# Performance work log

Hardware: AMD Instinct MI355X
Metric: run time of the kernel (lower is better)

The kernel has to match this reference:

```python
import jax, jax.numpy as jnp
import numpy as np

N = 50000   # nodes
E = 800000  # edges
C = 64      # num_channels
EPS = 1e-5


def setup_inputs() -> dict:
    key = jax.random.key(0)
    ks = jax.random.split(key, 12)
    x = jax.random.normal(ks[0], (N, C), dtype=jnp.float32)
    vec = jax.random.normal(ks[1], (N, 3, C), dtype=jnp.float32)
    senders = jax.random.randint(ks[2], (E,), 0, N, dtype=jnp.int32)
    receivers = jax.random.randint(ks[3], (E,), 0, N, dtype=jnp.int32)
    interaction_matrices = jax.random.normal(ks[4], (E, 3, 3), dtype=jnp.float32)
    # learned parameters
    ln_scale = jnp.ones((C,), dtype=jnp.float32)
    ln_bias = jnp.zeros((C,), dtype=jnp.float32)
    vln_weight = jnp.ones((C,), dtype=jnp.float32)  # VecLayerNorm weight (norm_type='none' -> identity norm, channel scale)
    w1 = jax.random.normal(ks[5], (C, 2 * C), dtype=jnp.float32) / np.sqrt(C)
    b1 = jnp.zeros((2 * C,), dtype=jnp.float32)
    w2 = jax.random.normal(ks[6], (2 * C, C), dtype=jnp.float32) / np.sqrt(2 * C)
    b2 = jnp.zeros((C,), dtype=jnp.float32)
    return {
        "x": x, "vec": vec, "senders": senders, "receivers": receivers,
        "interaction_matrices": interaction_matrices,
        "ln_scale": ln_scale, "ln_bias": ln_bias, "vln_weight": vln_weight,
        "w1": w1, "b1": b1, "w2": w2, "b2": b2,
    }


def reference(x, vec, senders, receivers, interaction_matrices,
              ln_scale, ln_bias, vln_weight, w1, b1, w2, b2):
    # LayerNorm(eps=1e-5) over channel dim
    mean = jnp.mean(x, axis=-1, keepdims=True)
    var = jnp.var(x, axis=-1, keepdims=True)
    x_norm = (x - mean) * jax.lax.rsqrt(var + EPS) * ln_scale + ln_bias
    # VecLayerNorm with norm_type='none': identity norm, learned per-channel weight
    vec_norm = vec * vln_weight  # [N, 3, C]
    # MLP: Dense(2C) -> silu -> Dense(C)
    p = jax.nn.silu(x_norm @ w1 + b1) @ w2 + b2  # [N, C]
    # gather to edges
    p_i = p[receivers]            # [E, C]
    p_j = p[senders]              # [E, C]
    vec_i = vec_norm[receivers]   # [E, 3, C]
    vec_j = vec_norm[senders]     # [E, 3, C]
    source_dipole = p_j[:, None, :] * vec_j                              # [E, 3, C]
    field_at_i = jnp.einsum('eij,ejc->eic', interaction_matrices, source_dipole)  # [E, 3, C]
    dEnergy = jnp.sum(p_i[:, None, :] * vec_i * field_at_i, axis=1)      # [E, C]
    dx = jax.ops.segment_sum(dEnergy, receivers, num_segments=x.shape[0])  # [N, C]
    return dx
```

## Files before the change

### kernel.cpp

```cpp
#include <hip/hip_runtime.h>

#define C 64
#define EPS 1e-5f
#define BUCK_CAP 1536
#define OVF_CAP 65536
#define SMASK 0x03ffffffu

typedef __attribute__((ext_vector_type(8))) short bf16x8;
typedef __attribute__((ext_vector_type(4))) float f32x4;

static __device__ __forceinline__ unsigned int f2bf(float f) {
  unsigned int x = __float_as_uint(f);
  return (x + 0x7fffu + ((x >> 16) & 1u)) >> 16;
}
static __device__ __forceinline__ float bflo2f(unsigned int p) {
  return __uint_as_float(p << 16);
}
static __device__ __forceinline__ float bfhi2f(unsigned int p) {
  return __uint_as_float(p & 0xffff0000u);
}

__global__ __launch_bounds__(256) void prep_weights(
    const float* __restrict__ w1, const float* __restrict__ w2,
    unsigned short* __restrict__ w1T, unsigned short* __restrict__ w2T) {
  int idx = blockIdx.x * 256 + threadIdx.x;
  if (idx < 2 * C * C) {
    int k = idx >> 6, c = idx & 63;
    w1T[idx] = (unsigned short)f2bf(w1[c * 2 * C + k]);
  } else if (idx < 4 * C * C) {
    int j = idx - 2 * C * C;
    int c = j >> 7, k = j & 127;
    w2T[j] = (unsigned short)f2bf(w2[k * C + c]);
  }
}

__global__ __launch_bounds__(256) void bin_kernel(
    const int* __restrict__ recv, const int* __restrict__ send,
    uint2* __restrict__ region, int* __restrict__ bucketCnt,
    int* __restrict__ ovfList, int* __restrict__ ovfCnt,
    int n_edges, int nbuck) {
  __shared__ int hist[1024];
  int t = threadIdx.x;
  for (int i = t; i < 1024; i += 256) hist[i] = 0;
  __syncthreads();

  int base = blockIdx.x * 4096;
  int myrecv[16], mysend[16];
#pragma unroll 16
  for (int j = 0; j < 16; j++) {
    int e = base + j * 256 + t;
    if (e < n_edges) {
      int r = recv[e];
      myrecv[j] = r;
      mysend[j] = send[e];
      atomicAdd(&hist[r >> 6], 1);
    } else {
      myrecv[j] = -1;
      mysend[j] = 0;
    }
  }
  __syncthreads();

  for (int i = t; i < nbuck; i += 256) {
    int c = hist[i];
    hist[i] = (c > 0) ? atomicAdd(&bucketCnt[i], c) : 0;
  }
  __syncthreads();

#pragma unroll 16
  for (int j = 0; j < 16; j++) {
    int r = myrecv[j];
    if (r >= 0) {
      int e = base + j * 256 + t;
      int b = r >> 6;
      int pos = atomicAdd(&hist[b], 1);
      if (pos < BUCK_CAP) {
        uint2 rec;
        rec.x = (unsigned)mysend[j] | ((unsigned)(r & 63) << 26);
        rec.y = (unsigned)e;
        region[(size_t)b * BUCK_CAP + pos] = rec;
      } else {
        int o = atomicAdd(ovfCnt, 1);
        if (o < OVF_CAP) ovfList[o] = e;
      }
    }
  }
}

__global__ __launch_bounds__(256) void sort_kernel(
    uint2* __restrict__ region, const int* __restrict__ bucketCnt,
    int* __restrict__ nodeBeg, int* __restrict__ nodeEnd, int n_nodes) {
  __shared__ uint2 buf[BUCK_CAP];
  __shared__ int hist[64];
  __shared__ int off[64];
  int b = blockIdx.x;
  int t = threadIdx.x;
  int cnt = bucketCnt[b];
  if (cnt > BUCK_CAP) cnt = BUCK_CAP;
  uint2* reg = region + (size_t)b * BUCK_CAP;

  if (t < 64) hist[t] = 0;
  __syncthreads();
  for (int i = t; i < cnt; i += 256) {
    uint2 r = reg[i];
    buf[i] = r;
    atomicAdd(&hist[r.x >> 26], 1);
  }
  __syncthreads();
  if (t == 0) {
    int run = 0;
#pragma unroll
    for (int j = 0; j < 64; j++) { off[j] = run; run += hist[j]; }
  }
  __syncthreads();
  for (int i = t; i < cnt; i += 256) {
    uint2 r = buf[i];
    int pos = atomicAdd(&off[r.x >> 26], 1);
    reg[pos] = r;
  }
  __syncthreads();
  if (t < 64) {
    int node = b * 64 + t;
    if (node < n_nodes) {
      int end = off[t];
      nodeBeg[node] = b * BUCK_CAP + (end - hist[t]);
      nodeEnd[node] = b * BUCK_CAP + end;
    }
  }
}

__global__ __launch_bounds__(256, 2) void node_kernel(
    const float* __restrict__ x, const float* __restrict__ vec,
    const float* __restrict__ ln_scale, const float* __restrict__ ln_bias,
    const float* __restrict__ vln_w,
    const unsigned short* __restrict__ w1T, const float* __restrict__ b1,
    const unsigned short* __restrict__ w2T, const float* __restrict__ b2,
    uint2* __restrict__ D16, int n_nodes) {
  __shared__ unsigned short An[64 * 72];
  __shared__ unsigned short Ss[64 * 136];
  __shared__ unsigned short W1s[128 * 72];
  __shared__ unsigned short W2s[64 * 136];

  const int t = threadIdx.x;
  const int lane = t & 63;
  const int wave = t >> 6;
  const int l15 = lane & 15;
  const int q = lane >> 4;

  {
    int r1 = t >> 1, h2 = t & 1;
    const uint4* s1 = (const uint4*)(w1T + r1 * 64 + h2 * 32);
    uint4* d1 = (uint4*)(W1s + r1 * 72 + h2 * 32);
    d1[0] = s1[0]; d1[1] = s1[1]; d1[2] = s1[2]; d1[3] = s1[3];
    int r2 = t >> 2, qd = t & 3;
    const uint4* s2 = (const uint4*)(w2T + r2 * 128 + qd * 32);
    uint4* d2 = (uint4*)(W2s + r2 * 136 + qd * 32);
    d2[0] = s2[0]; d2[1] = s2[1]; d2[2] = s2[2]; d2[3] = s2[3];
  }

  {
    int rowl = t >> 2;
    int part = t & 3;
    int node = blockIdx.x * 64 + rowl;
    int nc = node < n_nodes ? node : n_nodes - 1;
    const float* xp = x + (size_t)nc * C + part * 16;
    float xv[16];
    float s = 0.f;
#pragma unroll
    for (int i = 0; i < 4; i++) {
      float4 v = *(const float4*)(xp + i * 4);
      xv[i * 4 + 0] = v.x; xv[i * 4 + 1] = v.y;
      xv[i * 4 + 2] = v.z; xv[i * 4 + 3] = v.w;
      s += v.x + v.y + v.z + v.w;
    }
    s += __shfl_xor(s, 1);
    s += __shfl_xor(s, 2);
    float mean = s * (1.f / C);
    float vs = 0.f;
#pragma unroll
    for (int i = 0; i < 16; i++) {
      float d = xv[i] - mean;
      vs += d * d;
    }
    vs += __shfl_xor(vs, 1);
    vs += __shfl_xor(vs, 2);
    float rs = rsqrtf(vs * (1.f / C) + EPS);
    float ls[16], lb[16];
#pragma unroll
    for (int i = 0; i < 4; i++) {
      float4 a = *(const float4*)(ln_scale + part * 16 + i * 4);
      float4 b = *(const float4*)(ln_bias + part * 16 + i * 4);
      ls[i * 4 + 0] = a.x; ls[i * 4 + 1] = a.y; ls[i * 4 + 2] = a.z; ls[i * 4 + 3] = a.w;
      lb[i * 4 + 0] = b.x; lb[i * 4 + 1] = b.y; lb[i * 4 + 2] = b.z; lb[i * 4 + 3] = b.w;
    }
    unsigned int bp[8];
#pragma unroll
    for (int i = 0; i < 8; i++) {
      float e0 = (xv[2 * i] - mean) * rs * ls[2 * i] + lb[2 * i];
      float e1 = (xv[2 * i + 1] - mean) * rs * ls[2 * i + 1] + lb[2 * i + 1];
      bp[i] = f2bf(e0) | (f2bf(e1) << 16);
    }
    uint4* dst = (uint4*)(An + rowl * 72 + part * 16);
    uint4 p0 = {bp[0], bp[1], bp[2], bp[3]};
    uint4 p1 = {bp[4], bp[5], bp[6], bp[7]};
    dst[0] = p0;
    dst[1] = p1;
  }
  __syncthreads();

  const int Mbase = wave * 16;

  bf16x8 a0 = *(const bf16x8*)(An + (Mbase + l15) * 72 + q * 8);
  bf16x8 a1 = *(const bf16x8*)(An + (Mbase + l15) * 72 + 32 + q * 8);
  f32x4 acc1[8];
#pragma unroll
  for (int nt = 0; nt < 8; nt++) {
    const unsigned short* wb = W1s + (nt * 16 + l15) * 72 + q * 8;
    bf16x8 b0 = *(const bf16x8*)(wb);
    bf16x8 b1f = *(const bf16x8*)(wb + 32);
    f32x4 z = {0.f, 0.f, 0.f, 0.f};
    z = __builtin_amdgcn_mfma_f32_16x16x32_bf16(a0, b0, z, 0, 0, 0);
    z = __builtin_amdgcn_mfma_f32_16x16x32_bf16(a1, b1f, z, 0, 0, 0);
    acc1[nt] = z;
  }
#pragma unroll
  for (int nt = 0; nt < 8; nt++) {
    float bb = b1[nt * 16 + l15];
#pragma unroll
    for (int r = 0; r < 4; r++) {
      float h = acc1[nt][r] + bb;
      float sg = h / (1.f + __expf(-h));
      Ss[(Mbase + q * 4 + r) * 136 + nt * 16 + l15] = (unsigned short)f2bf(sg);
    }
  }
  __syncthreads();

  bf16x8 a2[4];
#pragma unroll
  for (int kt = 0; kt < 4; kt++)
    a2[kt] = *(const bf16x8*)(Ss + (Mbase + l15) * 136 + kt * 32 + q * 8);
  f32x4 acc2[4];
#pragma unroll
  for (int nt = 0; nt < 4; nt++) {
    f32x4 z = {0.f, 0.f, 0.f, 0.f};
#pragma unroll
    for (int kt = 0; kt < 4; kt++) {
      bf16x8 b = *(const bf16x8*)(W2s + (nt * 16 + l15) * 136 + kt * 32 + q * 8);
      z = __builtin_amdgcn_mfma_f32_16x16x32_bf16(a2[kt], b, z, 0, 0, 0);
    }
    acc2[nt] = z;
  }

#pragma unroll
  for (int nt = 0; nt < 4; nt++) {
    int cc = nt * 16 + l15;
    float bb = b2[cc];
    float vw = vln_w[cc];
#pragma unroll
    for (int r = 0; r < 4; r++) {
      int rl = Mbase + q * 4 + r;
      int nn = blockIdx.x * 64 + rl;
      if (nn < n_nodes) {
        float p = (acc2[nt][r] + bb) * vw;
        const float* vp = vec + (size_t)nn * (3 * C) + cc;
        float v0 = vp[0], v1 = vp[C], v2 = vp[2 * C];
        uint2 u;
        u.x = f2bf(p * v0) | (f2bf(p * v1) << 16);
        u.y = f2bf(p * v2);
        D16[(size_t)nn * C + cc] = u;
      }
    }
  }
}

__global__ __launch_bounds__(256) void accum_node(
    const uint2* __restrict__ region, const int* __restrict__ nodeBeg,
    const int* __restrict__ nodeEnd, const float* __restrict__ Mmat,
    const uint2* __restrict__ D2, float* __restrict__ dx, int n_nodes) {
  int wid = threadIdx.x >> 6;
  int lane = threadIdx.x & 63;
  int n = blockIdx.x * 4 + wid;
  if (n >= n_nodes) return;

  int beg = nodeBeg[n];
  int end = nodeEnd[n];

  uint2 dr = D2[(size_t)n * C + lane];
  float r0 = bflo2f(dr.x), r1 = bfhi2f(dr.x), r2 = bflo2f(dr.y);
  float acc = 0.f;

  if (beg < end) {
    const int last = end - 1;
    uint2 svA, svB, svC, svD;
    float mA[9], mB[9], mC[9], mD[9];

#define LOADSLOT(SV, MM, IDX)                                                \
  {                                                                          \
    uint2 rec_ = region[(IDX)];                                              \
    SV = D2[(size_t)(rec_.x & SMASK) * C + lane];                            \
    const float* Mp_ =                                                       \
        Mmat + (size_t)__builtin_amdgcn_readfirstlane((int)rec_.y) * 9;      \
    _Pragma("unroll") for (int j_ = 0; j_ < 9; j_++) MM[j_] = Mp_[j_];       \
  }

#define COMPUTE(SV, MM)                                                      \
  {                                                                          \
    float a0 = bflo2f(SV.x), a1 = bfhi2f(SV.x), a2 = bflo2f(SV.y);           \
    float f0 = MM[0] * a0 + MM[1] * a1 + MM[2] * a2;                         \
    float f1 = MM[3] * a0 + MM[4] * a1 + MM[5] * a2;                         \
    float f2 = MM[6] * a0 + MM[7] * a1 + MM[8] * a2;                         \
    acc += r0 * f0 + r1 * f1 + r2 * f2;                                      \
  }

    int i1 = (beg + 1 > last) ? last : beg + 1;
    int i2 = (beg + 2 > last) ? last : beg + 2;
    int i3 = (beg + 3 > last) ? last : beg + 3;
    LOADSLOT(svA, mA, beg)
    LOADSLOT(svB, mB, i1)
    LOADSLOT(svC, mC, i2)
    LOADSLOT(svD, mD, i3)

    for (int e = beg; e <= last; e += 4) {
#define STAGE(K, SV, MM)                                                     \
  if (e + (K) <= last) {                                                     \
    COMPUTE(SV, MM)                                                          \
    int nx = e + (K) + 4;                                                    \
    if (nx <= last) LOADSLOT(SV, MM, nx)                                     \
  }
      STAGE(0, svA, mA)
      STAGE(1, svB, mB)
      STAGE(2, svC, mC)
      STAGE(3, svD, mD)
#undef STAGE
    }
#undef LOADSLOT
#undef COMPUTE
  }
  dx[(size_t)n * C + lane] = acc;
}

__global__ __launch_bounds__(256) void fixup_kernel(
    const int* __restrict__ ovfList, const int* __restrict__ ovfCnt,
    const int* __restrict__ senders, const int* __restrict__ receivers,
    const float* __restrict__ Mmat, const uint2* __restrict__ D2,
    float* __restrict__ dx) {
  int nov = *ovfCnt;
  if (nov > OVF_CAP) nov = OVF_CAP;
  int lane = threadIdx.x & 63;
  for (int idx = blockIdx.x * 4 + (threadIdx.x >> 6); idx < nov;
       idx += gridDim.x * 4) {
    int e = ovfList[idx];
    int s = senders[e];
    int r = receivers[e];
    uint2 sv = D2[(size_t)s * C + lane];
    uint2 rv = D2[(size_t)r * C + lane];
    const float* M = Mmat + (size_t)e * 9;
    float a0 = bflo2f(sv.x), a1 = bfhi2f(sv.x), a2 = bflo2f(sv.y);
    float c0 = bflo2f(rv.x), c1 = bfhi2f(rv.x), c2 = bflo2f(rv.y);
    float f0 = M[0] * a0 + M[1] * a1 + M[2] * a2;
    float f1 = M[3] * a0 + M[4] * a1 + M[5] * a2;
    float f2 = M[6] * a0 + M[7] * a1 + M[8] * a2;
    float dE = c0 * f0 + c1 * f1 + c2 * f2;
    atomicAdd(dx + (size_t)r * C + lane, dE);
  }
}

extern "C" void kernel_launch(void* const* d_in, const int* in_sizes, int n_in,
                              void* d_out, int out_size, void* d_ws, size_t ws_size,
                              hipStream_t stream) {
  const float* x        = (const float*)d_in[0];
  const float* vec      = (const float*)d_in[1];
  const int*   senders  = (const int*)d_in[2];
  const int*   receivers= (const int*)d_in[3];
  const float* Mmat     = (const float*)d_in[4];
  const float* ln_scale = (const float*)d_in[5];
  const float* ln_bias  = (const float*)d_in[6];
  const float* vln_w    = (const float*)d_in[7];
  const float* w1       = (const float*)d_in[8];
  const float* b1       = (const float*)d_in[9];
  const float* w2       = (const float*)d_in[10];
  const float* b2       = (const float*)d_in[11];
  float* dx = (float*)d_out;

  int n_nodes = in_sizes[0] / C;
  int n_edges = in_sizes[2];
  int nbuck = (n_nodes + 63) >> 6;

  unsigned short* w1T = (unsigned short*)d_ws;
  unsigned short* w2T = w1T + 2 * C * C;
  uint2* D16 = (uint2*)((char*)d_ws + 32768);
  char* p = (char*)d_ws + 32768 + (size_t)n_nodes * C * sizeof(uint2);
  p = (char*)(((size_t)p + 255) & ~(size_t)255);
  int* cnts    = (int*)p;  p += (1024 + 1) * 4;
  p = (char*)(((size_t)p + 255) & ~(size_t)255);
  uint2* region = (uint2*)p;  p += (size_t)nbuck * BUCK_CAP * 8;
  int* nodeBeg = (int*)p;     p += (size_t)n_nodes * 4;
  int* nodeEnd = (int*)p;     p += (size_t)n_nodes * 4;
  int* ovfList = (int*)p;
  int* bucketCnt = cnts;
  int* ovfCnt = cnts + 1024;

  prep_weights<<<64, 256, 0, stream>>>(w1, w2, w1T, w2T);

  hipMemsetAsync(cnts, 0, (1024 + 1) * sizeof(int), stream);
  bin_kernel<<<(n_edges + 4095) / 4096, 256, 0, stream>>>(
      receivers, senders, region, bucketCnt, ovfList, ovfCnt, n_edges, nbuck);

  sort_kernel<<<nbuck, 256, 0, stream>>>(
      region, bucketCnt, nodeBeg, nodeEnd, n_nodes);

  node_kernel<<<(n_nodes + 63) / 64, 256, 0, stream>>>(
      x, vec, ln_scale, ln_bias, vln_w, w1T, b1, w2T, b2, D16, n_nodes);

  accum_node<<<(n_nodes + 3) / 4, 256, 0, stream>>>(
      region, nodeBeg, nodeEnd, Mmat, D16, dx, n_nodes);

  fixup_kernel<<<128, 256, 0, stream>>>(
      ovfList, ovfCnt, senders, receivers, Mmat, D16, dx);
}
```

Measured before the change: 301.8 us.

## Read MLP weights from global, raise occupancy, deepen accum prefetch pipeline

node_kernel no longer stages w1T/w2T into shared memory; MFMA B-operands are loaded straight from global (cached) memory, which removes the per-block copy and shrinks LDS so the launch bound can rise to 4 blocks per CU. accum_node makes the segment bounds wave-uniform via readfirstlane and deepens the software-pipelined edge prefetch from 4 to 6 slots to hide more gather latency. The costs are higher register pressure in accum_node and uncoalesced global weight reads in the node MLP.

```diff
diff --git a/kernel.cpp b/kernel.cpp
--- a/kernel.cpp
+++ b/kernel.cpp
@@ -129,7 +129,7 @@
   }
 }
 
-__global__ __launch_bounds__(256, 2) void node_kernel(
+__global__ __launch_bounds__(256, 4) void node_kernel(
     const float* __restrict__ x, const float* __restrict__ vec,
     const float* __restrict__ ln_scale, const float* __restrict__ ln_bias,
     const float* __restrict__ vln_w,
@@ -138,25 +138,12 @@
     uint2* __restrict__ D16, int n_nodes) {
   __shared__ unsigned short An[64 * 72];
   __shared__ unsigned short Ss[64 * 136];
-  __shared__ unsigned short W1s[128 * 72];
-  __shared__ unsigned short W2s[64 * 136];
 
   const int t = threadIdx.x;
   const int lane = t & 63;
   const int wave = t >> 6;
   const int l15 = lane & 15;
   const int q = lane >> 4;
-
-  {
-    int r1 = t >> 1, h2 = t & 1;
-    const uint4* s1 = (const uint4*)(w1T + r1 * 64 + h2 * 32);
-    uint4* d1 = (uint4*)(W1s + r1 * 72 + h2 * 32);
-    d1[0] = s1[0]; d1[1] = s1[1]; d1[2] = s1[2]; d1[3] = s1[3];
-    int r2 = t >> 2, qd = t & 3;
-    const uint4* s2 = (const uint4*)(w2T + r2 * 128 + qd * 32);
-    uint4* d2 = (uint4*)(W2s + r2 * 136 + qd * 32);
-    d2[0] = s2[0]; d2[1] = s2[1]; d2[2] = s2[2]; d2[3] = s2[3];
-  }
 
   {
     int rowl = t >> 2;
@@ -215,7 +202,7 @@
   f32x4 acc1[8];
 #pragma unroll
   for (int nt = 0; nt < 8; nt++) {
-    const unsigned short* wb = W1s + (nt * 16 + l15) * 72 + q * 8;
+    const unsigned short* wb = w1T + (nt * 16 + l15) * 64 + q * 8;
     bf16x8 b0 = *(const bf16x8*)(wb);
     bf16x8 b1f = *(const bf16x8*)(wb + 32);
     f32x4 z = {0.f, 0.f, 0.f, 0.f};
@@ -245,7 +232,7 @@
     f32x4 z = {0.f, 0.f, 0.f, 0.f};
 #pragma unroll
     for (int kt = 0; kt < 4; kt++) {
-      bf16x8 b = *(const bf16x8*)(W2s + (nt * 16 + l15) * 136 + kt * 32 + q * 8);
+      bf16x8 b = *(const bf16x8*)(w2T + (nt * 16 + l15) * 128 + kt * 32 + q * 8);
       z = __builtin_amdgcn_mfma_f32_16x16x32_bf16(a2[kt], b, z, 0, 0, 0);
     }
     acc2[nt] = z;
@@ -282,8 +269,8 @@
   int n = blockIdx.x * 4 + wid;
   if (n >= n_nodes) return;
 
-  int beg = nodeBeg[n];
-  int end = nodeEnd[n];
+  int beg = __builtin_amdgcn_readfirstlane(nodeBeg[n]);
+  int end = __builtin_amdgcn_readfirstlane(nodeEnd[n]);
 
   uint2 dr = D2[(size_t)n * C + lane];
   float r0 = bflo2f(dr.x), r1 = bfhi2f(dr.x), r2 = bflo2f(dr.y);
@@ -291,8 +278,8 @@
 
   if (beg < end) {
     const int last = end - 1;
-    uint2 svA, svB, svC, svD;
-    float mA[9], mB[9], mC[9], mD[9];
+    uint2 svA, svB, svC, svD, svE, svF;
+    float mA[9], mB[9], mC[9], mD[9], mE[9], mF[9];
 
 #define LOADSLOT(SV, MM, IDX)                                                \
   {                                                                          \
@@ -315,22 +302,28 @@
     int i1 = (beg + 1 > last) ? last : beg + 1;
     int i2 = (beg + 2 > last) ? last : beg + 2;
     int i3 = (beg + 3 > last) ? last : beg + 3;
+    int i4 = (beg + 4 > last) ? last : beg + 4;
+    int i5 = (beg + 5 > last) ? last : beg + 5;
     LOADSLOT(svA, mA, beg)
     LOADSLOT(svB, mB, i1)
     LOADSLOT(svC, mC, i2)
     LOADSLOT(svD, mD, i3)
-
-    for (int e = beg; e <= last; e += 4) {
+    LOADSLOT(svE, mE, i4)
+    LOADSLOT(svF, mF, i5)
+
+    for (int e = beg; e <= last; e += 6) {
 #define STAGE(K, SV, MM)                                                     \
   if (e + (K) <= last) {                                                     \
     COMPUTE(SV, MM)                                                          \
-    int nx = e + (K) + 4;                                                    \
+    int nx = e + (K) + 6;                                                    \
     if (nx <= last) LOADSLOT(SV, MM, nx)                                     \
   }
       STAGE(0, svA, mA)
       STAGE(1, svB, mB)
       STAGE(2, svC, mC)
       STAGE(3, svD, mD)
+      STAGE(4, svE, mE)
+      STAGE(5, svF, mF)
 #undef STAGE
     }
 #undef LOADSLOT
```

New measurement: 269.4 us. -10.7%, faster.
